# Kernel tuning notes

Measured on AMD Instinct MI355X. Metric: run time of the kernel, lower is better.

The kernel has to match this reference:

```python
import jax, jax.numpy as jnp
import numpy as np

B = 32
M = 3
MAG_DIM = 20
STD = 0.28
INV = float(1.0 / (np.sqrt(2.0) * STD))
NORM = float(1.0 / (np.sqrt(2.0 * np.pi) * STD))


def _lrelu(x):
    return jax.nn.leaky_relu(x, 0.01)


def _conv(x, w, b):
    y = jax.lax.conv_general_dilated(x, w, (2, 2), 'VALID',
                                     dimension_numbers=('NCHW', 'OIHW', 'NCHW'))
    return _lrelu(y + b[None, :, None, None])


def _combos(x):
    # x: [N, c, d] -> [N, c, c, 2d], pairs[n, i, j] = concat(x[n, i], x[n, j])
    # (matches torch getCombinations: tensorB = expand-over-i, tensorA = expand-over-j)
    N, c, d = x.shape
    left = jnp.broadcast_to(x[:, :, None, :], (N, c, c, d))
    right = jnp.broadcast_to(x[:, None, :, :], (N, c, c, d))
    return jnp.concatenate([left, right], axis=-1)


def _forward(batch, conv_w1, conv_b1, conv_w2, conv_b2, conv_w3, conv_b3, conv_w4, conv_b4,
             post_w, post_b, g_w1, g_b1, g_w2, g_b2, g_w3, g_b3, g_w4, g_b4,
             h_w1, h_b1, h_w2, h_b2, h_w3, h_b3, f_w1, f_b1, f_w2, f_b2, ff_w, ff_b):
    bsz = batch.shape[0]
    x = batch.reshape(bsz * 16, 1, 80, 80)
    # magnitude encoding (computed under no_grad in the original)
    mag = jnp.linspace(-1.0, 1.0, MAG_DIM).astype(batch.dtype)  # [20]
    t = jnp.tanh(x * (2.0 / 255.0) - 1.0)                        # [N,1,80,80]
    enc = NORM * jnp.exp(-(((t + mag[None, :, None, None]) * INV) ** 2))  # [N,20,80,80]
    enc = jax.lax.stop_gradient(enc)
    y = _conv(enc, conv_w1, conv_b1)   # [N,32,39,39]
    y = _conv(y, conv_w2, conv_b2)     # [N,32,19,19]
    y = _conv(y, conv_w3, conv_b3)     # [N,32,9,9]
    y = _conv(y, conv_w4, conv_b4)     # [N,32,4,4]
    obj = y.reshape(bsz * 16, 512) @ post_w + post_b             # [N,247]
    panel = obj.reshape(bsz, 16, 247)
    given, options = panel[:, :8], panel[:, 8:]
    giv = jnp.broadcast_to(given[:, None], (bsz, 8, 8, 247))
    ctx = jnp.concatenate([giv, options[:, :, None, :]], axis=2)  # [B,8,9,247]
    tags = jnp.broadcast_to(jnp.eye(9, dtype=batch.dtype), (bsz * 8, 9, 9))
    objects = jnp.concatenate([ctx.reshape(bsz * 8, 9, 247), tags], axis=-1)  # [B*8,9,256]

    z = _combos(objects).reshape(-1, 512)  # [B*8*81, 512]
    z = _lrelu(z @ g_w1 + g_b1)
    z = _lrelu(z @ g_w2 + g_b2)
    z = _lrelu(z @ g_w3 + g_b3)
    z = _lrelu(z @ g_w4 + g_b4)
    sum_j = z.reshape(bsz * 8, 9, 9, 256).sum(axis=2)  # [B*8,9,256]
    for i in range(h_w1.shape[0]):
        p = _combos(sum_j).reshape(-1, 512)
        z = _lrelu(p @ h_w1[i] + h_b1[i])
        z = _lrelu(z @ h_w2[i] + h_b2[i])
        z = _lrelu(z @ h_w3[i] + h_b3[i])
        sum_j = z.reshape(bsz * 8, 9, 9, 256).sum(axis=2)
    h_sum = sum_j.sum(axis=1)                          # [B*8,256]
    z = _lrelu(h_sum @ f_w1 + f_b1)
    z = _lrelu(z @ f_w2 + f_b2)
    result = z @ ff_w + ff_b                           # [B*8,1]
    answer = result.reshape(bsz, 8)
    loss = jnp.mean(h_sum ** 2) + jnp.mean(result ** 2)
    return answer, loss


def setup_inputs():
    key = jax.random.key(0)
    ks = iter(jax.random.split(key, 40))

    def U(shape, fan_in):
        s = 1.0 / np.sqrt(fan_in)
        return jax.random.uniform(next(ks), shape, jnp.float32, -s, s)

    inp = {
        'batch': jax.random.uniform(next(ks), (B, 16, 80, 80), jnp.float32, 0.0, 255.0),
        'conv_w1': U((32, MAG_DIM, 3, 3), MAG_DIM * 9), 'conv_b1': U((32,), MAG_DIM * 9),
        'conv_w2': U((32, 32, 3, 3), 288), 'conv_b2': U((32,), 288),
        'conv_w3': U((32, 32, 3, 3), 288), 'conv_b3': U((32,), 288),
        'conv_w4': U((32, 32, 3, 3), 288), 'conv_b4': U((32,), 288),
        'post_w': U((512, 247), 512), 'post_b': U((247,), 512),
        'g_w1': U((512, 512), 512), 'g_b1': U((512,), 512),
        'g_w2': U((512, 512), 512), 'g_b2': U((512,), 512),
        'g_w3': U((512, 512), 512), 'g_b3': U((512,), 512),
        'g_w4': U((512, 256), 512), 'g_b4': U((256,), 512),
        'h_w1': U((M, 512, 256), 512), 'h_b1': U((M, 256), 512),
        'h_w2': U((M, 256, 256), 256), 'h_b2': U((M, 256), 256),
        'h_w3': U((M, 256, 256), 256), 'h_b3': U((M, 256), 256),
        'f_w1': U((256, 256), 256), 'f_b1': U((256,), 256),
        'f_w2': U((256, 256), 256), 'f_b2': U((256,), 256),
        'ff_w': U((256, 1), 256), 'ff_b': U((1,), 256),
    }
    return inp


def reference(batch, conv_w1, conv_b1, conv_w2, conv_b2, conv_w3, conv_b3, conv_w4, conv_b4,
              post_w, post_b, g_w1, g_b1, g_w2, g_b2, g_w3, g_b3, g_w4, g_b4,
              h_w1, h_b1, h_w2, h_b2, h_w3, h_b3, f_w1, f_b1, f_w2, f_b2, ff_w, ff_b):
    return _forward(batch, conv_w1, conv_b1, conv_w2, conv_b2, conv_w3, conv_b3, conv_w4, conv_b4,
                    post_w, post_b, g_w1, g_b1, g_w2, g_b2, g_w3, g_b3, g_w4, g_b4,
                    h_w1, h_b1, h_w2, h_b2, h_w3, h_b3, f_w1, f_b1, f_w2, f_b2, ff_w, ff_b)
```

## Files before the change

### kernel.cpp

```cpp
#include <hip/hip_runtime.h>
#include <hip/hip_bf16.h>
#include <math.h>

static __device__ __forceinline__ float lrelu(float v){ return v > 0.0f ? v : 0.01f*v; }

static __device__ __forceinline__ unsigned short f2bf(float f){
  unsigned int u = __float_as_uint(f);
  unsigned int r = (u + 0x7fffu + ((u >> 16) & 1u)) >> 16;
  return (unsigned short)r;
}
static __device__ __forceinline__ float bf2f(unsigned short u){
  return __uint_as_float(((unsigned int)u) << 16);
}
static __device__ __forceinline__ unsigned int pack_bf2(float lo, float hi){
  __hip_bfloat162 bb = __float22bfloat162_rn(make_float2(lo, hi));
  return *reinterpret_cast<unsigned int*>(&bb);
}
static __device__ __forceinline__ void gload16(const void* g, void* l){
  __builtin_amdgcn_global_load_lds(
    (const __attribute__((address_space(1))) void*)(const void*)g,
    (__attribute__((address_space(3))) void*)l, 16, 0, 0);
}

#define ENC_NORM 1.4247939f
#define GC_C     6.3775511f
#define GC_2CD   1.3426423f
#define GC_CD2   0.070665395f
#define GC_S1    0.86820227f

typedef __attribute__((ext_vector_type(4))) float f32x4;
typedef __attribute__((ext_vector_type(8))) short bf16x8;

__global__ __launch_bounds__(256) void k_prep(
    const float* __restrict__ g_w1, const float* __restrict__ g_w2,
    const float* __restrict__ g_w3, const float* __restrict__ g_w4,
    const float* __restrict__ h_w1, const float* __restrict__ h_w2,
    const float* __restrict__ h_w3, const float* __restrict__ post_w,
    const float* __restrict__ conv_w2, const float* __restrict__ conv_w3,
    const float* __restrict__ conv_w4, const float* __restrict__ conv_w1,
    const float* __restrict__ f_w1, const float* __restrict__ f_w2,
    unsigned short* __restrict__ WT)
{
  int e = blockIdx.x*256 + threadIdx.x;
  float v;
  if (e < 262144) {
    int nn = e >> 8, kk = e & 255;
    v = (nn < 512) ? g_w1[kk*512 + nn] : g_w1[(256+kk)*512 + (nn-512)];
  } else if (e < 524288) {
    int r = e - 262144; int nn = r >> 9, kk = r & 511;
    v = g_w2[kk*512 + nn];
  } else if (e < 786432) {
    int r = e - 524288; int nn = r >> 9, kk = r & 511;
    v = g_w3[kk*512 + nn];
  } else if (e < 917504) {
    int r = e - 786432; int nn = r >> 9, kk = r & 511;
    v = g_w4[kk*256 + nn];
  } else if (e < 1310720) {
    int r = e - 917504; int i = r >> 17; int q = r & 131071;
    int nn = q >> 8, kk = q & 255;
    v = (nn < 256) ? h_w1[i*131072 + kk*256 + nn]
                   : h_w1[i*131072 + (256+kk)*256 + (nn-256)];
  } else if (e < 1507328) {
    int r = e - 1310720; int i = r >> 16; int q = r & 65535;
    int nn = q >> 8, kk = q & 255;
    v = h_w2[i*65536 + kk*256 + nn];
  } else if (e < 1703936) {
    int r = e - 1507328; int i = r >> 16; int q = r & 65535;
    int nn = q >> 8, kk = q & 255;
    v = h_w3[i*65536 + kk*256 + nn];
  } else if (e < 1835008) {
    int r = e - 1703936; int np = r >> 9, kp = r & 511;
    int px = kp >> 5, c = kp & 31;
    v = (np < 247) ? post_w[(c*16+px)*247 + np] : 0.f;
  } else if (e < 1862656) {
    int r = e - 1835008; int which = r / 9216; int q = r % 9216;
    int tap = q >> 10, o = (q >> 5) & 31, c = q & 31;
    const float* w = which==0 ? conv_w2 : (which==1 ? conv_w3 : conv_w4);
    v = w[(o*32+c)*9 + tap];
  } else if (e < 1871872) {
    int r = e - 1862656; int tap = r >> 10, o = (r >> 5) & 31, c = r & 31;
    v = (c < 20) ? conv_w1[(o*20+c)*9 + tap] : 0.f;
  } else if (e < 1937408) {
    int r = e - 1871872; int nn = r >> 8, kk = r & 255;
    v = f_w1[kk*256 + nn];
  } else {
    int r = e - 1937408; int nn = r >> 8, kk = r & 255;
    v = f_w2[kk*256 + nn];
  }
  WT[e] = f2bf(v);
}

__global__ __launch_bounds__(256, 1) void k_conv1m(
    const float* __restrict__ batch, const unsigned short* __restrict__ wc1,
    const float* __restrict__ bias, unsigned short* __restrict__ y)
{
  __shared__ unsigned short ench[7][41][40];
  int n = blockIdx.x;
  int h = blockIdx.y;
  int c0 = h * 40;
  int OWH = h ? 19 : 20;
  int owbase = h * 20;
  int tid = threadIdx.x;
  int lane = tid & 63, wid = tid >> 6;
  int lr = lane & 15, kg = lane >> 4;

  bf16x8 bf0[9], bf1[9];
  #pragma unroll
  for (int tap = 0; tap < 9; ++tap) {
    bf0[tap] = *(const bf16x8*)&wc1[tap*1024 + lr*32 + kg*8];
    bf1[tap] = *(const bf16x8*)&wc1[tap*1024 + (16+lr)*32 + kg*8];
  }
  float b0 = bias[lr], b1 = bias[16 + lr];
  const float S2 = GC_S1 * GC_S1;

  for (int s = 0; s < 13; ++s) {
    int orow0 = s * 3;
    int irow0 = orow0 * 2;
    const float* img = batch + (size_t)n*6400 + irow0*80;
    for (int p = tid; p < 7*41; p += 256) {
      int row = p / 41, hx = p % 41;
      int lc = (hx < 21) ? 2*hx : 2*(hx-21)+1;
      int c = c0 + lc;
      if (c > 78) continue;
      float x = img[row*80 + c];
      float E = __expf(x * (4.0f/255.0f) - 2.0f);
      float t = 1.0f - 2.0f*__builtin_amdgcn_rcpf(E + 1.0f);
      float z = t - 1.0f;
      float e = ENC_NORM * __expf(-GC_C*z*z);
      float rg = __expf(-GC_2CD*z - GC_CD2);
      unsigned int pk[16];
      #pragma unroll
      for (int cp = 0; cp < 10; ++cp) {
        float e1 = e * rg;
        pk[cp] = pack_bf2(e, e1);
        e  = e1 * rg * GC_S1;
        rg = rg * S2;
      }
      #pragma unroll
      for (int cp = 10; cp < 16; ++cp) pk[cp] = 0u;
      unsigned short* dst = &ench[row][hx][0];
      *(uint4*)(dst)      = *(uint4*)&pk[0];
      *(uint4*)(dst + 8)  = *(uint4*)&pk[4];
      *(uint4*)(dst + 16) = *(uint4*)&pk[8];
      *(uint4*)(dst + 24) = *(uint4*)&pk[12];
    }
    __syncthreads();

    int totpx = 3 * OWH;
    {
      int t = wid;
      int pa = t*16 + lr;
      int pc = (pa < totpx) ? pa : (totpx - 1);
      int ohl = pc / OWH, lw = pc % OWH;
      f32x4 acc0 = {0.f,0.f,0.f,0.f}, acc1 = {0.f,0.f,0.f,0.f};
      #pragma unroll
      for (int kh = 0; kh < 3; ++kh) {
        int r = ohl*2 + kh;
        #pragma unroll
        for (int kw = 0; kw < 3; ++kw) {
          int hidx = (kw == 1) ? (21 + lw) : (lw + (kw >> 1));
          bf16x8 a = *(const bf16x8*)&ench[r][hidx][kg*8];
          int tap = kh*3 + kw;
          acc0 = __builtin_amdgcn_mfma_f32_16x16x32_bf16(a, bf0[tap], acc0, 0, 0, 0);
          acc1 = __builtin_amdgcn_mfma_f32_16x16x32_bf16(a, bf1[tap], acc1, 0, 0, 0);
        }
      }
      #pragma unroll
      for (int rr = 0; rr < 4; ++rr) {
        int ps = t*16 + kg*4 + rr;
        if (ps < totpx) {
          int soh = orow0 + ps / OWH, sow = owbase + ps % OWH;
          unsigned short* op = y + (((size_t)n*39 + soh)*39 + sow)*32;
          op[lr]      = f2bf(lrelu(acc0[rr] + b0));
          op[16 + lr] = f2bf(lrelu(acc1[rr] + b1));
        }
      }
    }
    __syncthreads();
  }
}

template<int H, int W, int OH, int OW, int ROWS, int SLABS>
__global__ __launch_bounds__(256, 1) void k_cmfma(
    const unsigned short* __restrict__ in, const unsigned short* __restrict__ wc,
    const float* __restrict__ bias, unsigned short* __restrict__ out)
{
  constexpr int IR = 2*ROWS + 1;
  constexpr int EV = (W + 1) / 2;
  __shared__ unsigned short xs[IR][W][40];
  int n = blockIdx.x;
  int tid = threadIdx.x;
  int lane = tid & 63, wid = tid >> 6;
  int lr = lane & 15, kg = lane >> 4;

  bf16x8 bf0[9], bf1[9];
  #pragma unroll
  for (int tap = 0; tap < 9; ++tap) {
    bf0[tap] = *(const bf16x8*)&wc[(tap*32 + lr)*32      + kg*8];
    bf1[tap] = *(const bf16x8*)&wc[(tap*32 + 16 + lr)*32 + kg*8];
  }
  float b0 = bias[lr], b1 = bias[16 + lr];

  for (int s = 0; s < SLABS; ++s) {
    int orow0 = (blockIdx.y * SLABS + s) * ROWS;
    if (orow0 >= OH) break;
    int nrows = min(ROWS, OH - orow0);
    int irow0 = orow0 * 2;
    int ir = min(2*nrows + 1, H - irow0);

    const unsigned short* ip = in + ((size_t)n*H + irow0)*W*32;
    int npx = ir * W;
    for (int p = tid; p < npx; p += 256) {
      const uint4* src = (const uint4*)(ip + (size_t)p*32);
      uint4 v0 = src[0], v1 = src[1], v2 = src[2], v3 = src[3];
      int r = p / W, col = p % W;
      int hx = (col & 1) ? EV + (col >> 1) : (col >> 1);
      unsigned short* dst = &xs[r][hx][0];
      *(uint4*)(dst)      = v0;
      *(uint4*)(dst + 8)  = v1;
      *(uint4*)(dst + 16) = v2;
      *(uint4*)(dst + 24) = v3;
    }
    __syncthreads();

    int totpx = nrows * OW;
    int ntiles = (totpx + 15) >> 4;
    for (int t = wid; t < ntiles; t += 4) {
      int pa = t*16 + lr;
      int pc = (pa < totpx) ? pa : 0;
      int oh = pc / OW, ow = pc % OW;
      f32x4 acc0 = {0.f,0.f,0.f,0.f}, acc1 = {0.f,0.f,0.f,0.f};
      #pragma unroll
      for (int kh = 0; kh < 3; ++kh)
        #pragma unroll
        for (int kw = 0; kw < 3; ++kw) {
          int hidx = (kw == 1) ? (EV + ow) : (ow + (kw >> 1));
          bf16x8 a = *(const bf16x8*)&xs[oh*2 + kh][hidx][kg*8];
          acc0 = __builtin_amdgcn_mfma_f32_16x16x32_bf16(a, bf0[kh*3+kw], acc0, 0, 0, 0);
          acc1 = __builtin_amdgcn_mfma_f32_16x16x32_bf16(a, bf1[kh*3+kw], acc1, 0, 0, 0);
        }
      #pragma unroll
      for (int rr = 0; rr < 4; ++rr) {
        int ps = t*16 + kg*4 + rr;
        if (ps < totpx) {
          int soh = orow0 + ps / OW, sow = ps % OW;
          unsigned short* op = out + (((size_t)n*OH + soh)*OW + sow)*32;
          op[lr]      = f2bf(lrelu(acc0[rr] + b0));
          op[16 + lr] = f2bf(lrelu(acc1[rr] + b1));
        }
      }
    }
    __syncthreads();
  }
}

template<int OUT_BF16, int ACT>
__global__ __launch_bounds__(256) void k_mgemm(
    const unsigned short* __restrict__ A, const unsigned short* __restrict__ Wt,
    const float* __restrict__ bias, void* __restrict__ Cv,
    int M, int N, int K)
{
  __shared__ unsigned short As[128*64];
  __shared__ unsigned short Bs[128*64];
  int bm = blockIdx.x * 128;
  int bn = blockIdx.y * 128;
  int tid = threadIdx.x;
  int wid = tid >> 6, lane = tid & 63;
  int wr = (wid >> 1) * 64, wc = (wid & 1) * 64;
  int lr = lane & 15, kg = lane >> 4;

  int srow = lane >> 3;
  int ssw  = ((lane & 7) * 16) ^ (srow << 4);
  int rsw  = (lr & 7) << 4;

  f32x4 acc[4][4];
  #pragma unroll
  for (int i = 0; i < 4; ++i)
    #pragma unroll
    for (int j = 0; j < 4; ++j)
      acc[i][j] = (f32x4){0.f,0.f,0.f,0.f};

  for (int k0 = 0; k0 < K; k0 += 64) {
    #pragma unroll
    for (int i = 0; i < 4; ++i) {
      int rowc = wid*32 + i*8;
      int row  = rowc + srow;
      gload16((const char*)&A[(size_t)(bm + row)*K + k0] + ssw, &As[rowc*64]);
      gload16((const char*)&Wt[(size_t)(bn + row)*K + k0] + ssw, &Bs[rowc*64]);
    }
    __syncthreads();
    #pragma unroll
    for (int ks = 0; ks < 2; ++ks) {
      int roff = ((ks*64 + kg*16) ^ rsw) >> 1;
      bf16x8 a[4], b[4];
      #pragma unroll
      for (int i = 0; i < 4; ++i) {
        a[i] = *(const bf16x8*)&As[(wr + i*16 + lr)*64 + roff];
        b[i] = *(const bf16x8*)&Bs[(wc + i*16 + lr)*64 + roff];
      }
      #pragma unroll
      for (int i = 0; i < 4; ++i)
        #pragma unroll
        for (int j = 0; j < 4; ++j)
          acc[i][j] = __builtin_amdgcn_mfma_f32_16x16x32_bf16(a[i], b[j], acc[i][j], 0, 0, 0);
    }
    __syncthreads();
  }
  int r0 = (lane >> 4) * 4;
  #pragma unroll
  for (int i = 0; i < 4; ++i) {
    #pragma unroll
    for (int j = 0; j < 4; ++j) {
      int col = bn + wc + j*16 + lr;
      float bv = bias ? bias[col] : 0.f;
      #pragma unroll
      for (int rr = 0; rr < 4; ++rr) {
        int row = bm + wr + i*16 + r0 + rr;
        float v = acc[i][j][rr] + bv;
        if (ACT) v = lrelu(v);
        if (OUT_BF16) ((unsigned short*)Cv)[(size_t)row*N + col] = f2bf(v);
        else          ((float*)Cv)[(size_t)row*N + col] = v;
      }
    }
  }
}

__global__ __launch_bounds__(256) void k_pgemm(
    const unsigned short* __restrict__ UV, const unsigned short* __restrict__ Wt,
    const float* __restrict__ abias, const float* __restrict__ obias,
    unsigned short* __restrict__ C, int M, int N, int K)
{
  __shared__ unsigned short As[128*64];
  __shared__ unsigned short Bs[128*64];
  __shared__ float absm[512];
  int bm = blockIdx.x * 128;
  int bn = blockIdx.y * 128;
  int tid = threadIdx.x;
  int wid = tid >> 6, lane = tid & 63;
  int wr = (wid >> 1) * 64, wc = (wid & 1) * 64;
  int lr = lane & 15, kg = lane >> 4;
  int ld = 2*K;

  int srow = lane >> 3;
  int ssw  = ((lane & 7) * 16) ^ (srow << 4);
  int rsw  = (lr & 7) << 4;

  for (int idx = tid; idx < K; idx += 256) absm[idx] = abias[idx];

  int urow[4], vrow[4], arow[4], asw[4];
  #pragma unroll
  for (int i = 0; i < 4; ++i) {
    int ch = tid + (i << 8);
    int r = ch >> 3;
    int m = bm + r;
    int n = m / 81; int rem = m - n*81;
    int ii = rem / 9; int jj = rem - ii*9;
    urow[i] = n*9 + ii; vrow[i] = n*9 + jj;
    arow[i] = r;
    asw[i] = (((ch & 7) * 16) ^ ((r & 7) << 4)) >> 1;
  }
  __syncthreads();

  f32x4 acc[4][4];
  #pragma unroll
  for (int i = 0; i < 4; ++i)
    #pragma unroll
    for (int j = 0; j < 4; ++j)
      acc[i][j] = (f32x4){0.f,0.f,0.f,0.f};

  for (int k0 = 0; k0 < K; k0 += 64) {
    #pragma unroll
    for (int i = 0; i < 4; ++i) {
      int rowc = wid*32 + i*8;
      int row  = rowc + srow;
      gload16((const char*)&Wt[(size_t)(bn + row)*K + k0] + ssw, &Bs[rowc*64]);
    }
    #pragma unroll
    for (int i = 0; i < 4; ++i) {
      int ch = tid + (i << 8);
      int kc = (ch & 7) * 8;
      uint4 u4 = *(const uint4*)&UV[(size_t)urow[i]*ld + k0 + kc];
      uint4 v4 = *(const uint4*)&UV[(size_t)vrow[i]*ld + K + k0 + kc];
      const unsigned short* us = (const unsigned short*)&u4;
      const unsigned short* vs = (const unsigned short*)&v4;
      unsigned int pk[4];
      #pragma unroll
      for (int e2 = 0; e2 < 4; ++e2) {
        float a0 = bf2f(us[2*e2])   + bf2f(vs[2*e2])   + absm[k0 + kc + 2*e2];
        float a1 = bf2f(us[2*e2+1]) + bf2f(vs[2*e2+1]) + absm[k0 + kc + 2*e2+1];
        pk[e2] = pack_bf2(lrelu(a0), lrelu(a1));
      }
      *(uint4*)&As[arow[i]*64 + asw[i]] = *(uint4*)pk;
    }
    __syncthreads();
    #pragma unroll
    for (int ks = 0; ks < 2; ++ks) {
      int roff = ((ks*64 + kg*16) ^ rsw) >> 1;
      bf16x8 a[4], b[4];
      #pragma unroll
      for (int i = 0; i < 4; ++i) {
        a[i] = *(const bf16x8*)&As[(wr + i*16 + lr)*64 + roff];
        b[i] = *(const bf16x8*)&Bs[(wc + i*16 + lr)*64 + roff];
      }
      #pragma unroll
      for (int i = 0; i < 4; ++i)
        #pragma unroll
        for (int j = 0; j < 4; ++j)
          acc[i][j] = __builtin_amdgcn_mfma_f32_16x16x32_bf16(a[i], b[j], acc[i][j], 0, 0, 0);
    }
    __syncthreads();
  }
  int r0 = (lane >> 4) * 4;
  #pragma unroll
  for (int i = 0; i < 4; ++i) {
    #pragma unroll
    for (int j = 0; j < 4; ++j) {
      int col = bn + wc + j*16 + lr;
      float bv = obias[col];
      #pragma unroll
      for (int rr = 0; rr < 4; ++rr) {
        int row = bm + wr + i*16 + r0 + rr;
        C[(size_t)row*N + col] = f2bf(lrelu(acc[i][j][rr] + bv));
      }
    }
  }
}

__global__ void k_objects(const float* __restrict__ panel, const float* __restrict__ post_b,
                          unsigned short* __restrict__ obj)
{
  int idx = blockIdx.x*256 + threadIdx.x;
  int row = idx >> 8;
  int k = idx & 255;
  int slot = row % 9;
  int nn = row / 9;
  int b = nn >> 3, opt = nn & 7;
  float v;
  if (k < 247) {
    int src = (slot < 8) ? (b*16 + slot) : (b*16 + 8 + opt);
    v = panel[(size_t)src*256 + k] + post_b[k];
  } else {
    v = ((k - 247) == slot) ? 1.0f : 0.0f;
  }
  obj[idx] = f2bf(v);
}

__global__ void k_sumj(const unsigned short* __restrict__ Z, float* __restrict__ SJ,
                       unsigned short* __restrict__ SJb, int C)
{
  int idx = blockIdx.x*256 + threadIdx.x;
  int vpr = C >> 3;
  int orow = idx / vpr, kv = (idx - orow*vpr) << 3;
  int n = orow / 9, i = orow % 9;
  const unsigned short* base = Z + (size_t)(n*81 + i*9)*C + kv;
  float s[8];
  #pragma unroll
  for (int e = 0; e < 8; ++e) s[e] = 0.f;
  #pragma unroll
  for (int j = 0; j < 9; ++j) {
    bf16x8 v = *(const bf16x8*)(base + (size_t)j*C);
    #pragma unroll
    for (int e = 0; e < 8; ++e) s[e] += bf2f(((const unsigned short*)&v)[e]);
  }
  float* so = SJ + (size_t)orow*C + kv;
  #pragma unroll
  for (int e = 0; e < 8; ++e) so[e] = s[e];
  unsigned int pk[4];
  #pragma unroll
  for (int e2 = 0; e2 < 4; ++e2) pk[e2] = pack_bf2(s[2*e2], s[2*e2+1]);
  *(uint4*)(SJb + (size_t)orow*C + kv) = *(uint4*)pk;
}

__global__ void k_hsum(const float* __restrict__ SJ, float* __restrict__ HS,
                       unsigned short* __restrict__ HSb)
{
  int idx = blockIdx.x*256 + threadIdx.x;
  int n = idx >> 6, kc = (idx & 63) << 2;
  const float* base = SJ + (size_t)n*9*256 + kc;
  float4 s = {0.f,0.f,0.f,0.f};
  #pragma unroll
  for (int i = 0; i < 9; ++i) {
    float4 v = *(const float4*)(base + (size_t)i*256);
    s.x += v.x; s.y += v.y; s.z += v.z; s.w += v.w;
  }
  *(float4*)(HS + (size_t)n*256 + kc) = s;
  unsigned int pk[2];
  pk[0] = pack_bf2(s.x, s.y);
  pk[1] = pack_bf2(s.z, s.w);
  *(uint2*)(HSb + (size_t)n*256 + kc) = *(uint2*)pk;
}

__global__ __launch_bounds__(256) void k_tailfin(
    const float* __restrict__ HS, const unsigned short* __restrict__ F2,
    const float* __restrict__ ffw, const float* __restrict__ ffb,
    float* __restrict__ out)
{
  __shared__ float red[256];
  __shared__ float wsm[256];
  int tid = threadIdx.x;
  wsm[tid] = ffw[tid];
  float s = 0.f;
  for (int j = 0; j < 256; ++j) { float v = HS[j*256 + tid]; s += v*v; }
  red[tid] = s; __syncthreads();
  for (int off = 128; off > 0; off >>= 1) { if (tid < off) red[tid] += red[tid + off]; __syncthreads(); }
  float hsq = red[0];
  __syncthreads();
  float r = ffb[0];
  for (int k = 0; k < 256; ++k) r += bf2f(F2[(size_t)tid*256 + k])*wsm[k];
  red[tid] = r*r; __syncthreads();
  for (int off = 128; off > 0; off >>= 1) { if (tid < off) red[tid] += red[tid + off]; __syncthreads(); }
  out[tid] = r;
  if (tid == 0) out[256] = hsq/65536.0f + red[0]/256.0f;
}

extern "C" void kernel_launch(void* const* d_in, const int* in_sizes, int n_in,
                              void* d_out, int out_size, void* d_ws, size_t ws_size,
                              hipStream_t stream)
{
  const float* batch   = (const float*)d_in[0];
  const float* conv_w1 = (const float*)d_in[1];
  const float* conv_b1 = (const float*)d_in[2];
  const float* conv_w2 = (const float*)d_in[3];
  const float* conv_b2 = (const float*)d_in[4];
  const float* conv_w3 = (const float*)d_in[5];
  const float* conv_b3 = (const float*)d_in[6];
  const float* conv_w4 = (const float*)d_in[7];
  const float* conv_b4 = (const float*)d_in[8];
  const float* post_w  = (const float*)d_in[9];
  const float* post_b  = (const float*)d_in[10];
  const float* g_w1    = (const float*)d_in[11];
  const float* g_b1    = (const float*)d_in[12];
  const float* g_w2    = (const float*)d_in[13];
  const float* g_b2    = (const float*)d_in[14];
  const float* g_w3    = (const float*)d_in[15];
  const float* g_b3    = (const float*)d_in[16];
  const float* g_w4    = (const float*)d_in[17];
  const float* g_b4    = (const float*)d_in[18];
  const float* h_w1    = (const float*)d_in[19];
  const float* h_b1    = (const float*)d_in[20];
  const float* h_w2    = (const float*)d_in[21];
  const float* h_b2    = (const float*)d_in[22];
  const float* h_w3    = (const float*)d_in[23];
  const float* h_b3    = (const float*)d_in[24];
  const float* f_w1    = (const float*)d_in[25];
  const float* f_b1    = (const float*)d_in[26];
  const float* f_w2    = (const float*)d_in[27];
  const float* f_b2    = (const float*)d_in[28];
  const float* ff_w    = (const float*)d_in[29];
  const float* ff_b    = (const float*)d_in[30];

  char* wsb = (char*)d_ws;
  const size_t off_Y1    = 0;
  const size_t off_Y2    = 52000000;
  const size_t off_Y3    = 64000000;
  const size_t off_Y4    = 67000000;
  const size_t off_PANEL = 68000000;
  const size_t off_WT    = 132000000;
  const size_t off_Pb    = 0;
  const size_t off_Qb    = 22000000;
  const size_t off_UV    = 44000000;
  const size_t off_OBJb  = 54000000;
  const size_t off_SJ    = 56000000;
  const size_t off_SJb   = 59000000;
  const size_t off_HS    = 61000000;
  const size_t off_HSb   = 61500000;
  const size_t off_F1    = 62000000;
  const size_t off_F2    = 63000000;

  unsigned short* WT = (unsigned short*)(wsb + off_WT);
  const size_t wt_g1   = 0;
  const size_t wt_g2   = 262144;
  const size_t wt_g3   = 524288;
  const size_t wt_g4   = 786432;
  const size_t wt_h1   = 917504;
  const size_t wt_h2   = 1310720;
  const size_t wt_h3   = 1507328;
  const size_t wt_post = 1703936;
  const size_t wt_cw2  = 1835008;
  const size_t wt_cw3  = 1844224;
  const size_t wt_cw4  = 1853440;
  const size_t wt_cw1  = 1862656;
  const size_t wt_f1   = 1871872;
  const size_t wt_f2   = 1937408;

  dim3 b256(256);

  k_prep<<<dim3(7824), b256, 0, stream>>>(g_w1, g_w2, g_w3, g_w4, h_w1, h_w2, h_w3,
                                          post_w, conv_w2, conv_w3, conv_w4, conv_w1,
                                          f_w1, f_w2, WT);

  unsigned short* Y1 = (unsigned short*)(wsb + off_Y1);
  unsigned short* Y2 = (unsigned short*)(wsb + off_Y2);
  unsigned short* Y3 = (unsigned short*)(wsb + off_Y3);
  unsigned short* Y4 = (unsigned short*)(wsb + off_Y4);
  float* PANEL = (float*)(wsb + off_PANEL);

  k_conv1m<<<dim3(512,2), b256, 0, stream>>>(batch, WT + wt_cw1, conv_b1, Y1);
  k_cmfma<39,39,19,19, 5,2><<<dim3(512,2), b256, 0, stream>>>(Y1, WT + wt_cw2, conv_b2, Y2);
  k_cmfma<19,19, 9, 9, 9,1><<<dim3(512,1), b256, 0, stream>>>(Y2, WT + wt_cw3, conv_b3, Y3);
  k_cmfma< 9, 9, 4, 4, 4,1><<<dim3(512,1), b256, 0, stream>>>(Y3, WT + wt_cw4, conv_b4, Y4);

  k_mgemm<0,0><<<dim3(4,2), b256, 0, stream>>>(Y4, WT + wt_post, nullptr, PANEL, 512,256,512);

  unsigned short* OBJb = (unsigned short*)(wsb + off_OBJb);
  unsigned short* Pb   = (unsigned short*)(wsb + off_Pb);
  unsigned short* Qb   = (unsigned short*)(wsb + off_Qb);
  unsigned short* SJb  = (unsigned short*)(wsb + off_SJb);
  unsigned short* UVb  = (unsigned short*)(wsb + off_UV);
  float* SJ = (float*)(wsb + off_SJ);
  float* HS = (float*)(wsb + off_HS);
  unsigned short* HSb = (unsigned short*)(wsb + off_HSb);
  unsigned short* F1 = (unsigned short*)(wsb + off_F1);
  unsigned short* F2 = (unsigned short*)(wsb + off_F2);

  k_objects<<<dim3(2304), b256, 0, stream>>>(PANEL, post_b, OBJb);

  k_mgemm<1,0><<<dim3(18,8), b256, 0, stream>>>(OBJb, WT + wt_g1, nullptr, UVb, 2304,1024,256);
  k_pgemm<<<dim3(162,4), b256, 0, stream>>>(UVb, WT + wt_g2, g_b1, g_b2, Qb, 20736,512,512);
  k_mgemm<1,1><<<dim3(162,4), b256, 0, stream>>>(Qb, WT + wt_g3, g_b3, Pb, 20736,512,512);
  k_mgemm<1,1><<<dim3(162,2), b256, 0, stream>>>(Pb, WT + wt_g4, g_b4, Qb, 20736,256,512);
  k_sumj<<<dim3(288), b256, 0, stream>>>(Qb, SJ, SJb, 256);

  for (int i = 0; i < 3; ++i) {
    k_mgemm<1,0><<<dim3(18,4), b256, 0, stream>>>(SJb, WT + wt_h1 + (size_t)i*131072, nullptr, UVb, 2304,512,256);
    k_pgemm<<<dim3(162,2), b256, 0, stream>>>(UVb, WT + wt_h2 + (size_t)i*65536, h_b1 + i*256, h_b2 + i*256, Qb, 20736,256,256);
    k_mgemm<1,1><<<dim3(162,2), b256, 0, stream>>>(Qb, WT + wt_h3 + (size_t)i*65536, h_b3 + i*256, Pb, 20736,256,256);
    k_sumj<<<dim3(288), b256, 0, stream>>>(Pb, SJ, SJb, 256);
  }

  k_hsum<<<dim3(64), b256, 0, stream>>>(SJ, HS, HSb);
  k_mgemm<1,1><<<dim3(2,2), b256, 0, stream>>>(HSb, WT + wt_f1, f_b1, F1, 256,256,256);
  k_mgemm<1,1><<<dim3(2,2), b256, 0, stream>>>(F1,  WT + wt_f2, f_b2, F2, 256,256,256);
  k_tailfin<<<dim3(1), b256, 0, stream>>>(HS, F2, ff_w, ff_b, (float*)d_out);
}
```

Measured before the change: 340.4 us.

## Fuse conv3+conv4, fold object building into g1 GEMM, split conv1 rows

Fuses conv layers 3 and 4 into one kernel per image that keeps the conv3 output in shared memory, removing the Y3 round trip and one launch. Folds the object/tag construction (panel + post bias + one-hot tags) into the A-tile load of the first g GEMM, removing the k_objects kernel and the OBJb buffer. Splits conv1 over a third grid dimension covering row strips 0-6 and 7-12 to double block count. The fused conv34 runs conv4 on a single wave, so that part of the kernel has low parallelism.

After: 334.1 us. No clear change (-1.9%).

```diff
diff --git a/kernel.cpp b/kernel.cpp
--- a/kernel.cpp
+++ b/kernel.cpp
@@ -100,6 +100,8 @@
   int c0 = h * 40;
   int OWH = h ? 19 : 20;
   int owbase = h * 20;
+  int s0 = blockIdx.z * 7;
+  int s1 = blockIdx.z ? 13 : 7;
   int tid = threadIdx.x;
   int lane = tid & 63, wid = tid >> 6;
   int lr = lane & 15, kg = lane >> 4;
@@ -113,7 +115,7 @@
   float b0 = bias[lr], b1 = bias[16 + lr];
   const float S2 = GC_S1 * GC_S1;
 
-  for (int s = 0; s < 13; ++s) {
+  for (int s = s0; s < s1; ++s) {
     int orow0 = s * 3;
     int irow0 = orow0 * 2;
     const float* img = batch + (size_t)n*6400 + irow0*80;
@@ -254,6 +256,95 @@
   }
 }
 
+__global__ __launch_bounds__(256, 1) void k_conv34(
+    const unsigned short* __restrict__ in,
+    const unsigned short* __restrict__ wc3, const float* __restrict__ b3,
+    const unsigned short* __restrict__ wc4, const float* __restrict__ b4,
+    unsigned short* __restrict__ out)
+{
+  __shared__ unsigned short xs[19][19][40];
+  __shared__ unsigned short ys[9][9][40];
+  int n = blockIdx.x;
+  int tid = threadIdx.x;
+  int lane = tid & 63, wid = tid >> 6;
+  int lr = lane & 15, kg = lane >> 4;
+
+  bf16x8 c3a[9], c3b[9], c4a[9], c4b[9];
+  #pragma unroll
+  for (int tap = 0; tap < 9; ++tap) {
+    c3a[tap] = *(const bf16x8*)&wc3[(tap*32 + lr)*32      + kg*8];
+    c3b[tap] = *(const bf16x8*)&wc3[(tap*32 + 16 + lr)*32 + kg*8];
+    c4a[tap] = *(const bf16x8*)&wc4[(tap*32 + lr)*32      + kg*8];
+    c4b[tap] = *(const bf16x8*)&wc4[(tap*32 + 16 + lr)*32 + kg*8];
+  }
+  float b30 = b3[lr], b31 = b3[16+lr];
+  float b40 = b4[lr], b41 = b4[16+lr];
+
+  const unsigned short* ip = in + (size_t)n*19*19*32;
+  for (int p = tid; p < 361; p += 256) {
+    const uint4* src = (const uint4*)(ip + (size_t)p*32);
+    uint4 v0 = src[0], v1 = src[1], v2 = src[2], v3 = src[3];
+    int r = p / 19, col = p % 19;
+    int hx = (col & 1) ? 10 + (col >> 1) : (col >> 1);
+    unsigned short* dst = &xs[r][hx][0];
+    *(uint4*)(dst)      = v0;
+    *(uint4*)(dst + 8)  = v1;
+    *(uint4*)(dst + 16) = v2;
+    *(uint4*)(dst + 24) = v3;
+  }
+  __syncthreads();
+
+  for (int t = wid; t < 6; t += 4) {
+    int pa = t*16 + lr;
+    int pc = (pa < 81) ? pa : 0;
+    int oh = pc / 9, ow = pc % 9;
+    f32x4 acc0 = {0.f,0.f,0.f,0.f}, acc1 = {0.f,0.f,0.f,0.f};
+    #pragma unroll
+    for (int kh = 0; kh < 3; ++kh)
+      #pragma unroll
+      for (int kw = 0; kw < 3; ++kw) {
+        int hidx = (kw == 1) ? (10 + ow) : (ow + (kw >> 1));
+        bf16x8 a = *(const bf16x8*)&xs[oh*2 + kh][hidx][kg*8];
+        acc0 = __builtin_amdgcn_mfma_f32_16x16x32_bf16(a, c3a[kh*3+kw], acc0, 0, 0, 0);
+        acc1 = __builtin_amdgcn_mfma_f32_16x16x32_bf16(a, c3b[kh*3+kw], acc1, 0, 0, 0);
+      }
+    #pragma unroll
+    for (int rr = 0; rr < 4; ++rr) {
+      int ps = t*16 + kg*4 + rr;
+      if (ps < 81) {
+        int soh = ps / 9, sow = ps % 9;
+        int hx2 = (sow & 1) ? 5 + (sow >> 1) : (sow >> 1);
+        ys[soh][hx2][lr]      = f2bf(lrelu(acc0[rr] + b30));
+        ys[soh][hx2][16 + lr] = f2bf(lrelu(acc1[rr] + b31));
+      }
+    }
+  }
+  __syncthreads();
+
+  if (wid == 0) {
+    int pc = lr;
+    int oh = pc >> 2, ow = pc & 3;
+    f32x4 acc0 = {0.f,0.f,0.f,0.f}, acc1 = {0.f,0.f,0.f,0.f};
+    #pragma unroll
+    for (int kh = 0; kh < 3; ++kh)
+      #pragma unroll
+      for (int kw = 0; kw < 3; ++kw) {
+        int hidx = (kw == 1) ? (5 + ow) : (ow + (kw >> 1));
+        bf16x8 a = *(const bf16x8*)&ys[oh*2 + kh][hidx][kg*8];
+        acc0 = __builtin_amdgcn_mfma_f32_16x16x32_bf16(a, c4a[kh*3+kw], acc0, 0, 0, 0);
+        acc1 = __builtin_amdgcn_mfma_f32_16x16x32_bf16(a, c4b[kh*3+kw], acc1, 0, 0, 0);
+      }
+    #pragma unroll
+    for (int rr = 0; rr < 4; ++rr) {
+      int ps = kg*4 + rr;
+      int soh = ps >> 2, sow = ps & 3;
+      unsigned short* op = out + (((size_t)n*4 + soh)*4 + sow)*32;
+      op[lr]      = f2bf(lrelu(acc0[rr] + b40));
+      op[16 + lr] = f2bf(lrelu(acc1[rr] + b41));
+    }
+  }
+}
+
 template<int OUT_BF16, int ACT>
 __global__ __launch_bounds__(256) void k_mgemm(
     const unsigned short* __restrict__ A, const unsigned short* __restrict__ Wt,
@@ -426,23 +517,105 @@
   }
 }
 
-__global__ void k_objects(const float* __restrict__ panel, const float* __restrict__ post_b,
-                          unsigned short* __restrict__ obj)
-{
-  int idx = blockIdx.x*256 + threadIdx.x;
-  int row = idx >> 8;
-  int k = idx & 255;
-  int slot = row % 9;
-  int nn = row / 9;
-  int b = nn >> 3, opt = nn & 7;
-  float v;
-  if (k < 247) {
-    int src = (slot < 8) ? (b*16 + slot) : (b*16 + 8 + opt);
-    v = panel[(size_t)src*256 + k] + post_b[k];
-  } else {
-    v = ((k - 247) == slot) ? 1.0f : 0.0f;
-  }
-  obj[idx] = f2bf(v);
+__global__ __launch_bounds__(256) void k_g1o(
+    const float* __restrict__ panel, const float* __restrict__ post_b,
+    const unsigned short* __restrict__ Wt, unsigned short* __restrict__ C,
+    int M, int N, int K)
+{
+  __shared__ unsigned short As[128*64];
+  __shared__ unsigned short Bs[128*64];
+  __shared__ float pbs[256];
+  int bm = blockIdx.x * 128;
+  int bn = blockIdx.y * 128;
+  int tid = threadIdx.x;
+  int wid = tid >> 6, lane = tid & 63;
+  int wr = (wid >> 1) * 64, wc = (wid & 1) * 64;
+  int lr = lane & 15, kg = lane >> 4;
+
+  int srow = lane >> 3;
+  int ssw  = ((lane & 7) * 16) ^ (srow << 4);
+  int rsw  = (lr & 7) << 4;
+
+  if (tid < 256) pbs[tid] = (tid < 247) ? post_b[tid] : 0.f;
+
+  int srcr[4], slotr[4], arow[4], asw[4];
+  #pragma unroll
+  for (int i = 0; i < 4; ++i) {
+    int ch = tid + (i << 8);
+    int r = ch >> 3;
+    int m = bm + r;
+    int nn = m / 9; int sl = m - nn*9;
+    int b = nn >> 3, opt = nn & 7;
+    srcr[i] = (sl < 8) ? (b*16 + sl) : (b*16 + 8 + opt);
+    slotr[i] = sl;
+    arow[i] = r;
+    asw[i] = (((ch & 7) * 16) ^ ((r & 7) << 4)) >> 1;
+  }
+  __syncthreads();
+
+  f32x4 acc[4][4];
+  #pragma unroll
+  for (int i = 0; i < 4; ++i)
+    #pragma unroll
+    for (int j = 0; j < 4; ++j)
+      acc[i][j] = (f32x4){0.f,0.f,0.f,0.f};
+
+  for (int k0 = 0; k0 < K; k0 += 64) {
+    #pragma unroll
+    for (int i = 0; i < 4; ++i) {
+      int rowc = wid*32 + i*8;
+      int row  = rowc + srow;
+      gload16((const char*)&Wt[(size_t)(bn + row)*K + k0] + ssw, &Bs[rowc*64]);
+    }
+    #pragma unroll
+    for (int i = 0; i < 4; ++i) {
+      int ch = tid + (i << 8);
+      int kc = (ch & 7) * 8;
+      int kb = k0 + kc;
+      const float* pp = &panel[(size_t)srcr[i]*256 + kb];
+      unsigned int pk[4];
+      #pragma unroll
+      for (int e2 = 0; e2 < 4; ++e2) {
+        float v0 = pp[2*e2]   + pbs[kb + 2*e2];
+        float v1 = pp[2*e2+1] + pbs[kb + 2*e2+1];
+        int kk0 = kb + 2*e2, kk1 = kb + 2*e2 + 1;
+        if (kk0 >= 247) v0 = (kk0 - 247 == slotr[i]) ? 1.f : 0.f;
+        if (kk1 >= 247) v1 = (kk1 - 247 == slotr[i]) ? 1.f : 0.f;
+        pk[e2] = pack_bf2(v0, v1);
+      }
+      *(uint4*)&As[arow[i]*64 + asw[i]] = *(uint4*)pk;
+    }
+    __syncthreads();
+    #pragma unroll
+    for (int ks = 0; ks < 2; ++ks) {
+      int roff = ((ks*64 + kg*16) ^ rsw) >> 1;
+      bf16x8 a[4], b[4];
+      #pragma unroll
+      for (int i = 0; i < 4; ++i) {
+        a[i] = *(const bf16x8*)&As[(wr + i*16 + lr)*64 + roff];
+        b[i] = *(const bf16x8*)&Bs[(wc + i*16 + lr)*64 + roff];
+      }
+      #pragma unroll
+      for (int i = 0; i < 4; ++i)
+        #pragma unroll
+        for (int j = 0; j < 4; ++j)
+          acc[i][j] = __builtin_amdgcn_mfma_f32_16x16x32_bf16(a[i], b[j], acc[i][j], 0, 0, 0);
+    }
+    __syncthreads();
+  }
+  int r0 = (lane >> 4) * 4;
+  #pragma unroll
+  for (int i = 0; i < 4; ++i) {
+    #pragma unroll
+    for (int j = 0; j < 4; ++j) {
+      int col = bn + wc + j*16 + lr;
+      #pragma unroll
+      for (int rr = 0; rr < 4; ++rr) {
+        int row = bm + wr + i*16 + r0 + rr;
+        C[(size_t)row*N + col] = f2bf(acc[i][j][rr]);
+      }
+    }
+  }
 }
 
 __global__ void k_sumj(const unsigned short* __restrict__ Z, float* __restrict__ SJ,
@@ -552,14 +725,12 @@
   char* wsb = (char*)d_ws;
   const size_t off_Y1    = 0;
   const size_t off_Y2    = 52000000;
-  const size_t off_Y3    = 64000000;
   const size_t off_Y4    = 67000000;
   const size_t off_PANEL = 68000000;
   const size_t off_WT    = 132000000;
   const size_t off_Pb    = 0;
   const size_t off_Qb    = 22000000;
   const size_t off_UV    = 44000000;
-  const size_t off_OBJb  = 54000000;
   const size_t off_SJ    = 56000000;
   const size_t off_SJb   = 59000000;
   const size_t off_HS    = 61000000;
@@ -591,31 +762,26 @@
 
   unsigned short* Y1 = (unsigned short*)(wsb + off_Y1);
   unsigned short* Y2 = (unsigned short*)(wsb + off_Y2);
-  unsigned short* Y3 = (unsigned short*)(wsb + off_Y3);
   unsigned short* Y4 = (unsigned short*)(wsb + off_Y4);
   float* PANEL = (float*)(wsb + off_PANEL);
 
-  k_conv1m<<<dim3(512,2), b256, 0, stream>>>(batch, WT + wt_cw1, conv_b1, Y1);
-  k_cmfma<39,39,19,19, 5,2><<<dim3(512,2), b256, 0, stream>>>(Y1, WT + wt_cw2, conv_b2, Y2);
-  k_cmfma<19,19, 9, 9, 9,1><<<dim3(512,1), b256, 0, stream>>>(Y2, WT + wt_cw3, conv_b3, Y3);
-  k_cmfma< 9, 9, 4, 4, 4,1><<<dim3(512,1), b256, 0, stream>>>(Y3, WT + wt_cw4, conv_b4, Y4);
+  k_conv1m<<<dim3(512,2,2), b256, 0, stream>>>(batch, WT + wt_cw1, conv_b1, Y1);
+  k_cmfma<39,39,19,19,5,2><<<dim3(512,2), b256, 0, stream>>>(Y1, WT + wt_cw2, conv_b2, Y2);
+  k_conv34<<<dim3(512), b256, 0, stream>>>(Y2, WT + wt_cw3, conv_b3, WT + wt_cw4, conv_b4, Y4);
 
   k_mgemm<0,0><<<dim3(4,2), b256, 0, stream>>>(Y4, WT + wt_post, nullptr, PANEL, 512,256,512);
 
-  unsigned short* OBJb = (unsigned short*)(wsb + off_OBJb);
-  unsigned short* Pb   = (unsigned short*)(wsb + off_Pb);
-  unsigned short* Qb   = (unsigned short*)(wsb + off_Qb);
-  unsigned short* SJb  = (unsigned short*)(wsb + off_SJb);
-  unsigned short* UVb  = (unsigned short*)(wsb + off_UV);
+  unsigned short* Pb  = (unsigned short*)(wsb + off_Pb);
+  unsigned short* Qb  = (unsigned short*)(wsb + off_Qb);
+  unsigned short* UVb = (unsigned short*)(wsb + off_UV);
+  unsigned short* SJb = (unsigned short*)(wsb + off_SJb);
   float* SJ = (float*)(wsb + off_SJ);
   float* HS = (float*)(wsb + off_HS);
   unsigned short* HSb = (unsigned short*)(wsb + off_HSb);
   unsigned short* F1 = (unsigned short*)(wsb + off_F1);
   unsigned short* F2 = (unsigned short*)(wsb + off_F2);
 
-  k_objects<<<dim3(2304), b256, 0, stream>>>(PANEL, post_b, OBJb);
-
-  k_mgemm<1,0><<<dim3(18,8), b256, 0, stream>>>(OBJb, WT + wt_g1, nullptr, UVb, 2304,1024,256);
+  k_g1o<<<dim3(18,8), b256, 0, stream>>>(PANEL, post_b, WT + wt_g1, UVb, 2304,1024,256);
   k_pgemm<<<dim3(162,4), b256, 0, stream>>>(UVb, WT + wt_g2, g_b1, g_b2, Qb, 20736,512,512);
   k_mgemm<1,1><<<dim3(162,4), b256, 0, stream>>>(Qb, WT + wt_g3, g_b3, Pb, 20736,512,512);
   k_mgemm<1,1><<<dim3(162,2), b256, 0, stream>>>(Pb, WT + wt_g4, g_b4, Qb, 20736,256,512);
```
